# Kernel optimization log

Measured on AMD Instinct MI355X. Metric: run time of the kernel, lower is better.

Reference implementation:

```python
import jax, jax.numpy as jnp
import numpy as np


def _attention(q, k, v, causal):
    # q,k,v: (B, S, H, D) -> matches flash_attn_func input layout
    B, Sq, H, D = q.shape
    Sk = k.shape[1]
    scale = 1.0 / jnp.sqrt(jnp.asarray(D, dtype=q.dtype))
    # scores: (B, H, Sq, Sk)
    scores = jnp.einsum('bqhd,bkhd->bhqk', q, k) * scale
    if causal:
        # position i attends to j <= i (standard causal mask, Sq == Sk here)
        mask = jnp.tril(jnp.ones((Sq, Sk), dtype=bool))
        scores = jnp.where(mask[None, None], scores, jnp.asarray(-jnp.inf, dtype=scores.dtype))
    probs = jax.nn.softmax(scores, axis=-1)
    out = jnp.einsum('bhqk,bkhd->bqhd', probs, v)
    return out


def setup_inputs() -> dict:
    key = jax.random.key(0)
    kq, kk, kv = jax.random.split(key, 3)
    B, S, H, D = 2, 2048, 16, 128
    q = jax.random.normal(kq, (B, S, H, D), dtype=jnp.float32)
    k = jax.random.normal(kk, (B, S, H, D), dtype=jnp.float32)
    v = jax.random.normal(kv, (B, S, H, D), dtype=jnp.float32)
    return {"q": q, "k": k, "v": v, "causal": 1}


def reference(q, k, v, causal):
    return _attention(q, k, v, bool(causal))
```

## Files before the change

### kernel.cpp

```cpp
#include <hip/hip_runtime.h>

typedef short bf16x8 __attribute__((ext_vector_type(8)));
typedef float f32x16 __attribute__((ext_vector_type(16)));

constexpr int S = 2048;
constexpr int H = 16;
constexpr int D = 128;
constexpr int BM = 128;
constexpr int TILE = 8192;
constexpr int KSTR = 136;
constexpr int EPAD = 132;


__device__ inline unsigned int pk2(float a, float b) {
    unsigned int ua = __builtin_bit_cast(unsigned int, a);
    unsigned int ub = __builtin_bit_cast(unsigned int, b);
    ua += 0x7fffu + ((ua >> 16) & 1u);
    ub += 0x7fffu + ((ub >> 16) & 1u);
    return (ua >> 16) | (ub & 0xffff0000u);
}

__device__ __forceinline__ void gld16(const unsigned short* g, unsigned short* l) {
    __builtin_amdgcn_global_load_lds(
        (const __attribute__((address_space(1))) unsigned int*)g,
        (__attribute__((address_space(3))) unsigned int*)l, 16, 0, 0);
}

__global__ __launch_bounds__(256) void cvt_kv(const float* __restrict__ K,
                                              const float* __restrict__ V,
                                              unsigned short* __restrict__ Kb,
                                              unsigned short* __restrict__ Vtb) {
    __shared__ unsigned short Vl[64 * KSTR];
    const int tid = threadIdx.x;
    const int t   = blockIdx.x;
    const int bh  = blockIdx.y;
    const int b = bh >> 4, h = bh & 15;
    const size_t base = ((size_t)(b * S + t * 64) * H + h) * D;

    unsigned short* outK = Kb + ((size_t)bh * 32 + t) * TILE;
    #pragma unroll
    for (int u = 0; u < 4; ++u) {
        const int dlin = u * 256 + tid;
        const int grp = dlin >> 7;
        const int s   = dlin & 127;
        const int rho = s >> 4;
        const int c   = (s & 15) ^ rho;
        const float* p = K + base + (size_t)(grp * 8 + rho) * (H * D) + c * 8;
        float4 f0 = *(const float4*)p;
        float4 f1 = *(const float4*)(p + 4);
        unsigned int w[4];
        w[0] = pk2(f0.x, f0.y); w[1] = pk2(f0.z, f0.w);
        w[2] = pk2(f1.x, f1.y); w[3] = pk2(f1.z, f1.w);
        *(uint4*)(outK + dlin * 8) = *(const uint4*)w;
    }

    #pragma unroll
    for (int u = 0; u < 4; ++u) {
        const int cidx = tid + 256 * u;
        const int n    = cidx >> 4;
        const int off  = (cidx & 15) * 8;
        const float* p = V + base + (size_t)n * (H * D) + off;
        float4 f0 = *(const float4*)p;
        float4 f1 = *(const float4*)(p + 4);
        unsigned int w[4];
        w[0] = pk2(f0.x, f0.y); w[1] = pk2(f0.z, f0.w);
        w[2] = pk2(f1.x, f1.y); w[3] = pk2(f1.z, f1.w);
        *(uint4*)&Vl[n * KSTR + off] = *(const uint4*)w;
    }
    __syncthreads();

    const int d  = tid >> 1;
    const int kh = (tid & 1) * 32;
    unsigned short tmp[32];
    #pragma unroll
    for (int m = 0; m < 32; ++m) {
        const int sig = kh + m;
        const int k = (sig & ~12) | ((sig & 4) << 1) | ((sig & 8) >> 1);
        tmp[m] = Vl[k * KSTR + d];
    }
    unsigned short* outV = Vtb + ((size_t)bh * 32 + t) * TILE;
    const int g = d >> 3, rho = d & 7;
    #pragma unroll
    for (int uu = 0; uu < 4; ++uu) {
        const int cc = (kh >> 3) + uu;
        *(uint4*)(outV + g * 512 + (rho * 8 + (cc ^ rho)) * 8) = *(const uint4*)&tmp[uu * 8];
    }
}

__global__ __launch_bounds__(256, 2) void fa_fwd(
    const float* __restrict__ Q,
    const unsigned short* __restrict__ Kb,
    const unsigned short* __restrict__ Vtb,
    const int* __restrict__ causal_p,
    float* __restrict__ Op)
{
    __shared__ __align__(16) unsigned char smem[4 * 32 * EPAD * 4];
    unsigned short* KlB = (unsigned short*)smem;
    unsigned short* VtB = (unsigned short*)smem + 2 * TILE;

    const int tid  = threadIdx.x;
    const int wave = tid >> 6;
    const int lane = tid & 63;
    const int ln   = lane & 31;
    const int half = lane >> 5;

    int bh, qblk;
    if (gridDim.y == 32) {
        const int lid = blockIdx.x + (blockIdx.y << 4);
        const int xcd = lid & 7;
        const int ii  = lid >> 3;
        bh = (xcd << 2) + (ii & 3);
        const int qp = ii >> 2;
        qblk = (qp < 8) ? qp : 23 - qp;
    } else {
        bh = blockIdx.y;
        qblk = blockIdx.x;
    }
    const int b = bh >> 4;
    const int h = bh & 15;

    const int q0    = qblk * BM;
    const int qrow0 = q0 + wave * 32;
    const int causal = *causal_p;
    const float cfold = 0.12751743f;

    const unsigned short* Ksrc = Kb  + (size_t)bh * (32 * TILE);
    const unsigned short* Vsrc = Vtb + (size_t)bh * (32 * TILE);
    const int sg   = wave * 4;
    const int loff = lane * 8;

    #pragma unroll
    for (int qq = 0; qq < 4; ++qq)
        gld16(Ksrc + (sg + qq) * 512 + loff, KlB + (sg + qq) * 512);
    #pragma unroll
    for (int qq = 0; qq < 4; ++qq)
        gld16(Vsrc + (sg + qq) * 512 + loff, VtB + (sg + qq) * 512);

    bf16x8 qf[8];
    {
        const size_t rowoff = ((size_t)(b * S + qrow0 + ln) * H + h) * D;
        #pragma unroll
        for (int c = 0; c < 8; ++c) {
            float4 f0 = *(const float4*)(Q + rowoff + c * 16 + half * 8);
            float4 f1 = *(const float4*)(Q + rowoff + c * 16 + half * 8 + 4);
            unsigned int t[4];
            t[0] = pk2(f0.x * cfold, f0.y * cfold);
            t[1] = pk2(f0.z * cfold, f0.w * cfold);
            t[2] = pk2(f1.x * cfold, f1.y * cfold);
            t[3] = pk2(f1.z * cfold, f1.w * cfold);
            qf[c] = *(const bf16x8*)t;
        }
    }

    f32x16 o[4];
    #pragma unroll
    for (int dt = 0; dt < 4; ++dt)
        #pragma unroll
        for (int r = 0; r < 16; ++r) o[dt][r] = 0.0f;
    float l = 0.0f;

    const int jmax = causal ? ((q0 + BM - 1) >> 6) : (S / 64 - 1);

    const int kb   = (ln >> 3) * 1024 + (ln & 7) * 128;
    const int krho = ln & 7;
    const int vg   = (ln >> 3) * 512;
    const int vrho = ln & 7;

    asm volatile("s_waitcnt vmcnt(0)" ::: "memory");
    __builtin_amdgcn_s_barrier();

    int cur = 0;
    for (int j = 0; j <= jmax; ++j) {
        if (j < jmax) {
            const unsigned short* ks = Ksrc + (size_t)(j + 1) * TILE;
            const unsigned short* vs = Vsrc + (size_t)(j + 1) * TILE;
            unsigned short* kd = KlB + (cur ^ 1) * TILE;
            unsigned short* vd = VtB + (cur ^ 1) * TILE;
            #pragma unroll
            for (int qq = 0; qq < 4; ++qq)
                gld16(ks + (sg + qq) * 512 + loff, kd + (sg + qq) * 512);
            #pragma unroll
            for (int qq = 0; qq < 4; ++qq)
                gld16(vs + (sg + qq) * 512 + loff, vd + (sg + qq) * 512);
        }

        const bool active = (!causal) || (j * 64 <= qrow0 + 31);
        if (active) {
            const unsigned short* Klc = KlB + cur * TILE;
            const unsigned short* Vtc = VtB + cur * TILE;

            f32x16 sacc[2];
            __builtin_amdgcn_s_setprio(1);
            #pragma unroll
            for (int nt = 0; nt < 2; ++nt) {
                #pragma unroll
                for (int r = 0; r < 16; ++r) sacc[nt][r] = 0.0f;
                const unsigned short* kl = Klc + nt * 4096 + kb;
                #pragma unroll
                for (int c = 0; c < 8; ++c) {
                    uint4 raw = *(const uint4*)(kl + (((2 * c + half) ^ krho) << 3));
                    bf16x8 kf = *(const bf16x8*)&raw;
                    sacc[nt] = __builtin_amdgcn_mfma_f32_32x32x16_bf16(kf, qf[c], sacc[nt], 0, 0, 0);
                }
            }
            __builtin_amdgcn_s_setprio(0);

            float p[32];
            const int thr  = qrow0 + ln - j * 64;
            const bool full = (!causal) || (j * 64 + 63 <= qrow0);
            #pragma unroll
            for (int nt = 0; nt < 2; ++nt)
                #pragma unroll
                for (int r = 0; r < 16; ++r) {
                    float e = __builtin_amdgcn_exp2f(sacc[nt][r]);
                    if (!full) {
                        const int kl_ = nt * 32 + (r & 3) + 8 * (r >> 2) + 4 * half;
                        if (kl_ > thr) e = 0.0f;
                    }
                    l += e;
                    p[nt * 16 + r] = e;
                }

            __builtin_amdgcn_s_setprio(1);
            #pragma unroll
            for (int win = 0; win < 4; ++win) {
                unsigned int pw[4];
                #pragma unroll
                for (int d2 = 0; d2 < 4; ++d2)
                    pw[d2] = pk2(p[win * 8 + 2 * d2], p[win * 8 + 2 * d2 + 1]);
                bf16x8 pf = *(const bf16x8*)pw;
                const int voff = ((vrho * 8) + ((win * 2 + half) ^ vrho)) << 3;
                #pragma unroll
                for (int dt = 0; dt < 4; ++dt) {
                    uint4 raw = *(const uint4*)(Vtc + dt * 2048 + vg + voff);
                    bf16x8 vf = *(const bf16x8*)&raw;
                    o[dt] = __builtin_amdgcn_mfma_f32_32x32x16_bf16(vf, pf, o[dt], 0, 0, 0);
                }
            }
            __builtin_amdgcn_s_setprio(0);
        }

        asm volatile("s_waitcnt vmcnt(0)" ::: "memory");
        __builtin_amdgcn_s_barrier();
        cur ^= 1;
    }

    const float lt  = l + __shfl_xor(l, 32);
    const float inv = 1.0f / lt;
    float* sc = (float*)smem + wave * (32 * EPAD);
    #pragma unroll
    for (int dt = 0; dt < 4; ++dt)
        #pragma unroll
        for (int r = 0; r < 16; ++r) {
            const int d = dt * 32 + (r & 3) + 8 * (r >> 2) + 4 * half;
            sc[ln * EPAD + d] = o[dt][r] * inv;
        }
    __syncthreads();
    const int row = tid >> 1;
    const int dh  = (tid & 1) * 64;
    const float* s2 = (float*)smem + (row >> 5) * (32 * EPAD) + (row & 31) * EPAD + dh;
    float* op = Op + ((size_t)(b * S + q0 + row) * H + h) * D + dh;
    #pragma unroll
    for (int u = 0; u < 16; ++u)
        *(float4*)(op + u * 4) = *(const float4*)(s2 + u * 4);
}

extern "C" void kernel_launch(void* const* d_in, const int* in_sizes, int n_in,
                              void* d_out, int out_size, void* d_ws, size_t ws_size,
                              hipStream_t stream) {
    const int B = in_sizes[0] / (S * H * D);
    unsigned short* Kb  = (unsigned short*)d_ws;
    unsigned short* Vtb = Kb + (size_t)B * S * H * D;

    cvt_kv<<<dim3(S / 64, B * H), 256, 0, stream>>>(
        (const float*)d_in[1], (const float*)d_in[2], Kb, Vtb);
    fa_fwd<<<dim3(S / BM, B * H), 256, 0, stream>>>(
        (const float*)d_in[0], Kb, Vtb, (const int*)d_in[3], (float*)d_out);
}
```

Before: 201.0 us.

## Pair causal Q-blocks per workgroup with triple-buffered K/V prefetch

Each workgroup now handles two query blocks (qp and 15-qp) in sequence, which balances causal work per block and halves the grid to 256 workgroups. K/V staging moves from double to triple buffering with a two-tile-ahead prefetch and partial vmcnt waits. The LDS-staged output transpose is replaced by direct float4 stores from registers, and the s_setprio hints are removed. Launch bounds drop to one block per SIMD-occupancy hint, trading occupancy for a deeper pipeline and more LDS.

```diff
diff --git a/kernel.cpp b/kernel.cpp
--- a/kernel.cpp
+++ b/kernel.cpp
@@ -9,7 +9,6 @@
 constexpr int BM = 128;
 constexpr int TILE = 8192;
 constexpr int KSTR = 136;
-constexpr int EPAD = 132;
 
 
 __device__ inline unsigned int pk2(float a, float b) {
@@ -87,16 +86,15 @@
     }
 }
 
-__global__ __launch_bounds__(256, 2) void fa_fwd(
+__global__ __launch_bounds__(256, 1) void fa_fwd(
     const float* __restrict__ Q,
     const unsigned short* __restrict__ Kb,
     const unsigned short* __restrict__ Vtb,
     const int* __restrict__ causal_p,
     float* __restrict__ Op)
 {
-    __shared__ __align__(16) unsigned char smem[4 * 32 * EPAD * 4];
-    unsigned short* KlB = (unsigned short*)smem;
-    unsigned short* VtB = (unsigned short*)smem + 2 * TILE;
+    __shared__ unsigned short Kl[3][TILE];
+    __shared__ unsigned short Vl[3][TILE];
 
     const int tid  = threadIdx.x;
     const int wave = tid >> 6;
@@ -104,23 +102,19 @@
     const int ln   = lane & 31;
     const int half = lane >> 5;
 
-    int bh, qblk;
-    if (gridDim.y == 32) {
-        const int lid = blockIdx.x + (blockIdx.y << 4);
+    int bh, qp;
+    if (gridDim.x == 8 && gridDim.y == 32) {
+        const int lid = blockIdx.x + (blockIdx.y << 3);
         const int xcd = lid & 7;
         const int ii  = lid >> 3;
         bh = (xcd << 2) + (ii & 3);
-        const int qp = ii >> 2;
-        qblk = (qp < 8) ? qp : 23 - qp;
+        qp = ii >> 2;
     } else {
         bh = blockIdx.y;
-        qblk = blockIdx.x;
+        qp = blockIdx.x;
     }
     const int b = bh >> 4;
     const int h = bh & 15;
-
-    const int q0    = qblk * BM;
-    const int qrow0 = q0 + wave * 32;
     const int causal = *causal_p;
     const float cfold = 0.12751743f;
 
@@ -129,140 +123,142 @@
     const int sg   = wave * 4;
     const int loff = lane * 8;
 
-    #pragma unroll
-    for (int qq = 0; qq < 4; ++qq)
-        gld16(Ksrc + (sg + qq) * 512 + loff, KlB + (sg + qq) * 512);
-    #pragma unroll
-    for (int qq = 0; qq < 4; ++qq)
-        gld16(Vsrc + (sg + qq) * 512 + loff, VtB + (sg + qq) * 512);
-
-    bf16x8 qf[8];
-    {
-        const size_t rowoff = ((size_t)(b * S + qrow0 + ln) * H + h) * D;
-        #pragma unroll
-        for (int c = 0; c < 8; ++c) {
-            float4 f0 = *(const float4*)(Q + rowoff + c * 16 + half * 8);
-            float4 f1 = *(const float4*)(Q + rowoff + c * 16 + half * 8 + 4);
-            unsigned int t[4];
-            t[0] = pk2(f0.x * cfold, f0.y * cfold);
-            t[1] = pk2(f0.z * cfold, f0.w * cfold);
-            t[2] = pk2(f1.x * cfold, f1.y * cfold);
-            t[3] = pk2(f1.z * cfold, f1.w * cfold);
-            qf[c] = *(const bf16x8*)t;
-        }
-    }
-
-    f32x16 o[4];
-    #pragma unroll
-    for (int dt = 0; dt < 4; ++dt)
-        #pragma unroll
-        for (int r = 0; r < 16; ++r) o[dt][r] = 0.0f;
-    float l = 0.0f;
-
-    const int jmax = causal ? ((q0 + BM - 1) >> 6) : (S / 64 - 1);
-
     const int kb   = (ln >> 3) * 1024 + (ln & 7) * 128;
     const int krho = ln & 7;
     const int vg   = (ln >> 3) * 512;
     const int vrho = ln & 7;
 
-    asm volatile("s_waitcnt vmcnt(0)" ::: "memory");
-    __builtin_amdgcn_s_barrier();
-
-    int cur = 0;
-    for (int j = 0; j <= jmax; ++j) {
-        if (j < jmax) {
-            const unsigned short* ks = Ksrc + (size_t)(j + 1) * TILE;
-            const unsigned short* vs = Vsrc + (size_t)(j + 1) * TILE;
-            unsigned short* kd = KlB + (cur ^ 1) * TILE;
-            unsigned short* vd = VtB + (cur ^ 1) * TILE;
+    #pragma unroll 1
+    for (int ph = 0; ph < 2; ++ph) {
+        const int qblk  = ph ? (15 - qp) : qp;
+        const int q0    = qblk * BM;
+        const int qrow0 = q0 + wave * 32;
+        const int jmax  = causal ? ((q0 + BM - 1) >> 6) : (S / 64 - 1);
+
+        bf16x8 qf[8];
+        {
+            const size_t rowoff = ((size_t)(b * S + qrow0 + ln) * H + h) * D;
             #pragma unroll
-            for (int qq = 0; qq < 4; ++qq)
-                gld16(ks + (sg + qq) * 512 + loff, kd + (sg + qq) * 512);
+            for (int c = 0; c < 8; ++c) {
+                float4 f0 = *(const float4*)(Q + rowoff + c * 16 + half * 8);
+                float4 f1 = *(const float4*)(Q + rowoff + c * 16 + half * 8 + 4);
+                unsigned int t[4];
+                t[0] = pk2(f0.x * cfold, f0.y * cfold);
+                t[1] = pk2(f0.z * cfold, f0.w * cfold);
+                t[2] = pk2(f1.x * cfold, f1.y * cfold);
+                t[3] = pk2(f1.z * cfold, f1.w * cfold);
+                qf[c] = *(const bf16x8*)t;
+            }
+        }
+
+        #pragma unroll
+        for (int qq = 0; qq < 4; ++qq) {
+            gld16(Ksrc + (sg + qq) * 512 + loff, &Kl[0][(sg + qq) * 512]);
+            gld16(Vsrc + (sg + qq) * 512 + loff, &Vl[0][(sg + qq) * 512]);
+        }
+        #pragma unroll
+        for (int qq = 0; qq < 4; ++qq) {
+            gld16(Ksrc + TILE + (sg + qq) * 512 + loff, &Kl[1][(sg + qq) * 512]);
+            gld16(Vsrc + TILE + (sg + qq) * 512 + loff, &Vl[1][(sg + qq) * 512]);
+        }
+        asm volatile("s_waitcnt vmcnt(8)" ::: "memory");
+        __builtin_amdgcn_s_barrier();
+
+        f32x16 o[4];
+        #pragma unroll
+        for (int dt = 0; dt < 4; ++dt)
             #pragma unroll
-            for (int qq = 0; qq < 4; ++qq)
-                gld16(vs + (sg + qq) * 512 + loff, vd + (sg + qq) * 512);
-        }
-
-        const bool active = (!causal) || (j * 64 <= qrow0 + 31);
-        if (active) {
-            const unsigned short* Klc = KlB + cur * TILE;
-            const unsigned short* Vtc = VtB + cur * TILE;
-
-            f32x16 sacc[2];
-            __builtin_amdgcn_s_setprio(1);
+            for (int r = 0; r < 16; ++r) o[dt][r] = 0.0f;
+        float l = 0.0f;
+
+        int cur = 0;
+        #pragma unroll 1
+        for (int j = 0; j <= jmax; ++j) {
+            const bool pf2 = (j + 2 <= jmax);
+            if (pf2) {
+                int nxt = cur + 2; if (nxt >= 3) nxt -= 3;
+                const unsigned short* ks = Ksrc + (size_t)(j + 2) * TILE;
+                const unsigned short* vs = Vsrc + (size_t)(j + 2) * TILE;
+                #pragma unroll
+                for (int qq = 0; qq < 4; ++qq) {
+                    gld16(ks + (sg + qq) * 512 + loff, &Kl[nxt][(sg + qq) * 512]);
+                    gld16(vs + (sg + qq) * 512 + loff, &Vl[nxt][(sg + qq) * 512]);
+                }
+            }
+
+            const bool active = (!causal) || (j * 64 <= qrow0 + 31);
+            if (active) {
+                const unsigned short* Klc = Kl[cur];
+                const unsigned short* Vtc = Vl[cur];
+
+                f32x16 sacc[2];
+                #pragma unroll
+                for (int nt = 0; nt < 2; ++nt) {
+                    #pragma unroll
+                    for (int r = 0; r < 16; ++r) sacc[nt][r] = 0.0f;
+                    const unsigned short* kl = Klc + nt * 4096 + kb;
+                    #pragma unroll
+                    for (int c = 0; c < 8; ++c) {
+                        uint4 raw = *(const uint4*)(kl + (((2 * c + half) ^ krho) << 3));
+                        bf16x8 kf = *(const bf16x8*)&raw;
+                        sacc[nt] = __builtin_amdgcn_mfma_f32_32x32x16_bf16(kf, qf[c], sacc[nt], 0, 0, 0);
+                    }
+                }
+
+                float p[32];
+                const int thr  = qrow0 + ln - j * 64;
+                const bool full = (!causal) || (j * 64 + 63 <= qrow0);
+                #pragma unroll
+                for (int nt = 0; nt < 2; ++nt)
+                    #pragma unroll
+                    for (int r = 0; r < 16; ++r) {
+                        float e = __builtin_amdgcn_exp2f(sacc[nt][r]);
+                        if (!full) {
+                            const int kl_ = nt * 32 + (r & 3) + 8 * (r >> 2) + 4 * half;
+                            if (kl_ > thr) e = 0.0f;
+                        }
+                        l += e;
+                        p[nt * 16 + r] = e;
+                    }
+
+                #pragma unroll
+                for (int win = 0; win < 4; ++win) {
+                    unsigned int pw[4];
+                    #pragma unroll
+                    for (int d2 = 0; d2 < 4; ++d2)
+                        pw[d2] = pk2(p[win * 8 + 2 * d2], p[win * 8 + 2 * d2 + 1]);
+                    bf16x8 pf = *(const bf16x8*)pw;
+                    const int voff = ((vrho * 8) + ((win * 2 + half) ^ vrho)) << 3;
+                    #pragma unroll
+                    for (int dt = 0; dt < 4; ++dt) {
+                        uint4 raw = *(const uint4*)(Vtc + dt * 2048 + vg + voff);
+                        bf16x8 vf = *(const bf16x8*)&raw;
+                        o[dt] = __builtin_amdgcn_mfma_f32_32x32x16_bf16(vf, pf, o[dt], 0, 0, 0);
+                    }
+                }
+            }
+
+            if (pf2) asm volatile("s_waitcnt vmcnt(8)" ::: "memory");
+            else     asm volatile("s_waitcnt vmcnt(0)" ::: "memory");
+            __builtin_amdgcn_s_barrier();
+            cur += 1; if (cur >= 3) cur -= 3;
+        }
+
+        const float lt  = l + __shfl_xor(l, 32);
+        const float inv = 1.0f / lt;
+        float* op = Op + ((size_t)(b * S + qrow0 + ln) * H + h) * D;
+        #pragma unroll
+        for (int dt = 0; dt < 4; ++dt)
             #pragma unroll
-            for (int nt = 0; nt < 2; ++nt) {
-                #pragma unroll
-                for (int r = 0; r < 16; ++r) sacc[nt][r] = 0.0f;
-                const unsigned short* kl = Klc + nt * 4096 + kb;
-                #pragma unroll
-                for (int c = 0; c < 8; ++c) {
-                    uint4 raw = *(const uint4*)(kl + (((2 * c + half) ^ krho) << 3));
-                    bf16x8 kf = *(const bf16x8*)&raw;
-                    sacc[nt] = __builtin_amdgcn_mfma_f32_32x32x16_bf16(kf, qf[c], sacc[nt], 0, 0, 0);
-                }
-            }
-            __builtin_amdgcn_s_setprio(0);
-
-            float p[32];
-            const int thr  = qrow0 + ln - j * 64;
-            const bool full = (!causal) || (j * 64 + 63 <= qrow0);
-            #pragma unroll
-            for (int nt = 0; nt < 2; ++nt)
-                #pragma unroll
-                for (int r = 0; r < 16; ++r) {
-                    float e = __builtin_amdgcn_exp2f(sacc[nt][r]);
-                    if (!full) {
-                        const int kl_ = nt * 32 + (r & 3) + 8 * (r >> 2) + 4 * half;
-                        if (kl_ > thr) e = 0.0f;
-                    }
-                    l += e;
-                    p[nt * 16 + r] = e;
-                }
-
-            __builtin_amdgcn_s_setprio(1);
-            #pragma unroll
-            for (int win = 0; win < 4; ++win) {
-                unsigned int pw[4];
-                #pragma unroll
-                for (int d2 = 0; d2 < 4; ++d2)
-                    pw[d2] = pk2(p[win * 8 + 2 * d2], p[win * 8 + 2 * d2 + 1]);
-                bf16x8 pf = *(const bf16x8*)pw;
-                const int voff = ((vrho * 8) + ((win * 2 + half) ^ vrho)) << 3;
-                #pragma unroll
-                for (int dt = 0; dt < 4; ++dt) {
-                    uint4 raw = *(const uint4*)(Vtc + dt * 2048 + vg + voff);
-                    bf16x8 vf = *(const bf16x8*)&raw;
-                    o[dt] = __builtin_amdgcn_mfma_f32_32x32x16_bf16(vf, pf, o[dt], 0, 0, 0);
-                }
-            }
-            __builtin_amdgcn_s_setprio(0);
-        }
-
-        asm volatile("s_waitcnt vmcnt(0)" ::: "memory");
-        __builtin_amdgcn_s_barrier();
-        cur ^= 1;
-    }
-
-    const float lt  = l + __shfl_xor(l, 32);
-    const float inv = 1.0f / lt;
-    float* sc = (float*)smem + wave * (32 * EPAD);
-    #pragma unroll
-    for (int dt = 0; dt < 4; ++dt)
-        #pragma unroll
-        for (int r = 0; r < 16; ++r) {
-            const int d = dt * 32 + (r & 3) + 8 * (r >> 2) + 4 * half;
-            sc[ln * EPAD + d] = o[dt][r] * inv;
-        }
-    __syncthreads();
-    const int row = tid >> 1;
-    const int dh  = (tid & 1) * 64;
-    const float* s2 = (float*)smem + (row >> 5) * (32 * EPAD) + (row & 31) * EPAD + dh;
-    float* op = Op + ((size_t)(b * S + q0 + row) * H + h) * D + dh;
-    #pragma unroll
-    for (int u = 0; u < 16; ++u)
-        *(float4*)(op + u * 4) = *(const float4*)(s2 + u * 4);
+            for (int rq = 0; rq < 4; ++rq) {
+                float4 st;
+                st.x = o[dt][rq * 4 + 0] * inv;
+                st.y = o[dt][rq * 4 + 1] * inv;
+                st.z = o[dt][rq * 4 + 2] * inv;
+                st.w = o[dt][rq * 4 + 3] * inv;
+                *(float4*)(op + dt * 32 + 8 * rq + 4 * half) = st;
+            }
+    }
 }
 
 extern "C" void kernel_launch(void* const* d_in, const int* in_sizes, int n_in,
@@ -274,6 +270,6 @@
 
     cvt_kv<<<dim3(S / 64, B * H), 256, 0, stream>>>(
         (const float*)d_in[1], (const float*)d_in[2], Kb, Vtb);
-    fa_fwd<<<dim3(S / BM, B * H), 256, 0, stream>>>(
+    fa_fwd<<<dim3(8, B * H), 256, 0, stream>>>(
         (const float*)d_in[0], Kb, Vtb, (const int*)d_in[3], (float*)d_out);
 }
```

Result: no change. 202.4 us (+0.7%).
